# Kernel optimization log

Measured on AMD Instinct MI355X. Metric: run time of the kernel, lower is better.

## Reference

```python
import jax, jax.numpy as jnp
import numpy as np

N = 21  # nodes per graph (20 laser sectors + 1 robot node)
MAX_RANGE = 10.0
_bound = np.linspace(-np.pi / 2 - 0.03, np.pi / 2, 21, dtype=np.float32)[:-1]
_angles = _bound + np.float32(np.pi / 20)
ANGLE_FEAT = jnp.asarray(np.stack([np.sin(_angles), np.cos(_angles)], 1), dtype=jnp.float32)  # [20,2]


def _build_nodes(state24):
    # state24: [B,24] -> node features [B,21,7]
    B = state24.shape[0]
    laser = state24[:, :20, None] / MAX_RANGE                       # [B,20,1]
    angle = jnp.broadcast_to(ANGLE_FEAT[None], (B, 20, 2))          # [B,20,2]
    sector = jnp.concatenate([laser, angle, jnp.zeros((B, 20, 4), state24.dtype)], -1)  # [B,20,7]
    robot = jnp.concatenate([jnp.zeros((B, 1, 3), state24.dtype), state24[:, None, 20:]], -1)  # [B,1,7]
    return jnp.concatenate([sector, robot], axis=1)                 # [B,21,7]


def _gatv2(x, Wl, Wr, att, bias, heads, dim):
    # GATv2 over a fully-connected graph with self-loops (dense all-pairs).
    # e_ij = att . leaky_relu(Wl x_j + Wr x_i); alpha = softmax_j; out_i = sum_j alpha_ij (Wl x_j)
    B = x.shape[0]
    gl = (x @ Wl).reshape(B, N, heads, dim)  # source transform [B,j,H,D]
    gr = (x @ Wr).reshape(B, N, heads, dim)  # target transform [B,i,H,D]
    s = jax.nn.leaky_relu(gl[:, None] + gr[:, :, None], negative_slope=0.2)  # [B,i,j,H,D]
    e = jnp.einsum('bijhd,hd->bijh', s, att)                                  # [B,i,j,H]
    alpha = jax.nn.softmax(e, axis=2)                                          # softmax over sources j
    out = jnp.einsum('bijh,bjhd->bihd', alpha, gl).reshape(B, N, heads * dim)
    return out + bias


def setup_inputs() -> dict:
    key = jax.random.key(0)
    ks = jax.random.split(key, 16)
    r = lambda k, shape, s: (jax.random.normal(k, shape, dtype=jnp.float32) * s)
    B = 1024
    return {
        'state24': jax.random.normal(ks[0], (B, 24), dtype=jnp.float32),
        'Wl1': r(ks[1], (7, 256), 0.3), 'Wr1': r(ks[2], (7, 256), 0.3),
        'att1': r(ks[3], (4, 64), 0.1), 'b1': r(ks[4], (256,), 0.02),
        'Wl2': r(ks[5], (256, 64), 0.06), 'Wr2': r(ks[6], (256, 64), 0.06),
        'att2': r(ks[7], (1, 64), 0.1), 'b2': r(ks[8], (64,), 0.02),
        'fc1_w': r(ks[9], (64, 256), 0.12), 'fc1_b': r(ks[10], (256,), 0.02),
        'fc2_w': r(ks[11], (256, 256), 0.06), 'fc2_b': r(ks[12], (256,), 0.02),
        'fc3_w': r(ks[13], (256, 2), 0.06), 'fc3_b': r(ks[14], (2,), 0.02),
    }


def reference(state24, Wl1, Wr1, att1, b1, Wl2, Wr2, att2, b2,
              fc1_w, fc1_b, fc2_w, fc2_b, fc3_w, fc3_b):
    x = _build_nodes(state24)                               # [B,21,7]
    h = jax.nn.elu(_gatv2(x, Wl1, Wr1, att1, b1, 4, 64))    # [B,21,256]
    h = _gatv2(h, Wl2, Wr2, att2, b2, 1, 64)                # [B,21,64]
    nfv = jnp.mean(h, axis=1)                               # global_mean_pool -> [B,64]
    h = jax.nn.relu(nfv @ fc1_w + fc1_b)
    h = jax.nn.relu(h @ fc2_w + fc2_b)
    return jnp.tanh(h @ fc3_w + fc3_b)                      # [B,2]
```

## Files before the change

### kernel.cpp

```cpp
#include <hip/hip_runtime.h>
#include <hip/hip_fp16.h>
#include <math.h>

#define PI_D 3.141592653589793

typedef _Float16 h2 __attribute__((ext_vector_type(2)));
typedef _Float16 h4 __attribute__((ext_vector_type(4)));
typedef _Float16 h8 __attribute__((ext_vector_type(8)));
typedef unsigned short us8 __attribute__((ext_vector_type(8)));
typedef __fp16 f16v2 __attribute__((ext_vector_type(2)));
typedef __fp16 f16v8 __attribute__((ext_vector_type(8)));
typedef float f32x4 __attribute__((ext_vector_type(4)));

#define STR1 264
#define STR2H 72

#define SV(v, a, b) __builtin_shufflevector(v, v, a, b)

static __device__ __forceinline__ h2 pack_h2(float a, float b) {
    return __builtin_bit_cast(h2, __builtin_amdgcn_cvt_pkrtz(a, b));
}

static __device__ __forceinline__ float fdot2(h2 a, h2 b, float c) {
    return __builtin_amdgcn_fdot2(__builtin_bit_cast(f16v2, a),
                                  __builtin_bit_cast(f16v2, b), c, false);
}

static __device__ __forceinline__ h8 habs8(h8 x) {
    us8 u = __builtin_bit_cast(us8, x);
    us8 m = {0x7fff, 0x7fff, 0x7fff, 0x7fff, 0x7fff, 0x7fff, 0x7fff, 0x7fff};
    return __builtin_bit_cast(h8, (us8)(u & m));
}

static __device__ __forceinline__ f32x4 mfma16(h8 a, h8 b, f32x4 c) {
    return __builtin_amdgcn_mfma_f32_16x16x32_f16(
        __builtin_bit_cast(f16v8, a), __builtin_bit_cast(f16v8, b), c, 0, 0, 0);
}

static __device__ __forceinline__ void wave_fence() {
    asm volatile("" ::: "memory");
#if __has_builtin(__builtin_amdgcn_wave_barrier)
    __builtin_amdgcn_wave_barrier();
#endif
    asm volatile("" ::: "memory");
}

__global__ __launch_bounds__(256) void pack_weights_kernel(
    const float* __restrict__ Wl2, const float* __restrict__ Wr2,
    const float* __restrict__ fc1_w, const float* __restrict__ fc2_w,
    h8* __restrict__ ws)
{
    int idx = blockIdx.x * 256 + threadIdx.x;
    if (idx < 4096) {
        const float* W = idx < 2048 ? Wl2 : Wr2;
        int t = idx & 2047;
        int ntile = t >> 9, rem = t & 511;
        int kchunk = rem >> 6, lane = rem & 63;
        int n = ntile * 16 + (lane & 15);
        int k0 = kchunk * 32 + (lane >> 4) * 8;
        h8 o;
        #pragma unroll
        for (int j = 0; j < 8; ++j) o[j] = (_Float16)W[(k0 + j) * 64 + n];
        ws[idx] = o;
    } else if (idx < 6144) {
        int t = idx - 4096;
        int k2 = t >> 6, c = t & 63;
        h8 o;
        #pragma unroll
        for (int q = 0; q < 4; ++q) {
            o[2 * q]     = (_Float16)fc1_w[(2 * k2) * 256 + 4 * c + q];
            o[2 * q + 1] = (_Float16)fc1_w[(2 * k2 + 1) * 256 + 4 * c + q];
        }
        ws[idx] = o;
    } else {
        int t = idx - 6144;
        int k2 = t >> 6, c = t & 63;
        h8 o;
        #pragma unroll
        for (int q = 0; q < 4; ++q) {
            o[2 * q]     = (_Float16)fc2_w[(2 * k2) * 256 + 4 * c + q];
            o[2 * q + 1] = (_Float16)fc2_w[(2 * k2 + 1) * 256 + 4 * c + q];
        }
        ws[idx] = o;
    }
}

__global__ __launch_bounds__(256, 4) void actor_fused_kernel(
    const float* __restrict__ state24,
    const float* __restrict__ Wl1, const float* __restrict__ Wr1,
    const float* __restrict__ att1, const float* __restrict__ b1,
    const float* __restrict__ att2, const float* __restrict__ b2,
    const float* __restrict__ fc1_b, const float* __restrict__ fc2_b,
    const float* __restrict__ fc3_w, const float* __restrict__ fc3_b,
    const h8* __restrict__ wsL, const h8* __restrict__ wsR,
    const h8* __restrict__ wsF1, const h8* __restrict__ wsF2,
    float* __restrict__ out, int B)
{
    const int bix = blockIdx.x;
    if (bix >= B) return;
    const int tid = threadIdx.x;

    __shared__ float sinL[20], cosL[20], laserL[20], robotL[4];
    __shared__ __align__(16) h2 attLh[128];
    __shared__ __align__(16) h2 att2Lh[32];
    __shared__ __align__(16) _Float16 gr1h[22 * STR1];
    __shared__ __align__(16) union {
        struct { _Float16 gl1h[22 * STR1];
                 float ePf[128 * 24];
                 float uv[168]; } p1;
        struct { _Float16 gl2h[21 * STR2H];
                 _Float16 gr2h[21 * STR2H];
                 _Float16 gl2hT[64 * 32];
                 float e2[32 * 24];
                 float u2v2[42];
                 float red[4][256];
                 _Float16 nfvh[64]; _Float16 hah[256]; _Float16 hbh[256]; } p2;
    } U;

    if (tid < 20) {
        double step = (PI_D + 0.03) / 20.0;
        float bound = (float)(-PI_D / 2.0 - 0.03 + (double)tid * step);
        float ang = bound + (float)(PI_D / 20.0);
        sinL[tid] = sinf(ang);
        cosL[tid] = cosf(ang);
        laserL[tid] = state24[bix * 24 + tid] * 0.1f;
    }
    if (tid >= 32 && tid < 36) robotL[tid - 32] = state24[bix * 24 + 20 + (tid - 32)];
    if (tid < 128) {
        float2 ap = ((const float2*)att1)[tid];
        attLh[tid] = pack_h2(0.4f * ap.x, 0.4f * ap.y);
    }
    if (tid >= 128 && tid < 160) {
        float2 ap = ((const float2*)att2)[tid - 128];
        att2Lh[tid - 128] = pack_h2(0.4f * ap.x, 0.4f * ap.y);
    }
    __syncthreads();

    {
        const int h = tid >> 6;
        const int lane = tid & 63;

        {
            const int cp = lane & 31;
            const int half = lane >> 5;
            const int d2 = h * 32 + cp;
            float2 wl[7], wr[7];
            #pragma unroll
            for (int k = 0; k < 7; k++) {
                wl[k] = ((const float2*)Wl1)[k * 128 + d2];
                wr[k] = ((const float2*)Wr1)[k * 128 + d2];
            }
            if (half == 0) {
                h2 zz2 = {};
                ((h2*)(U.p1.gl1h + 21 * STR1))[d2] = zz2;
                ((h2*)(gr1h + 21 * STR1))[d2] = zz2;
            }
            const int base = half * 11;
            #pragma unroll
            for (int nn = 0; nn < 11; ++nn) {
                int node = base + nn;
                if (node < 21) {
                    float a0, a1, b0, b1v;
                    if (node < 20) {
                        float l = laserL[node], s = sinL[node], c = cosL[node];
                        a0 = l * wl[0].x + s * wl[1].x + c * wl[2].x;
                        a1 = l * wl[0].y + s * wl[1].y + c * wl[2].y;
                        b0 = l * wr[0].x + s * wr[1].x + c * wr[2].x;
                        b1v = l * wr[0].y + s * wr[1].y + c * wr[2].y;
                    } else {
                        float r0 = robotL[0], r1 = robotL[1], r2 = robotL[2], r3 = robotL[3];
                        a0 = r0 * wl[3].x + r1 * wl[4].x + r2 * wl[5].x + r3 * wl[6].x;
                        a1 = r0 * wl[3].y + r1 * wl[4].y + r2 * wl[5].y + r3 * wl[6].y;
                        b0 = r0 * wr[3].x + r1 * wr[4].x + r2 * wr[5].x + r3 * wr[6].x;
                        b1v = r0 * wr[3].y + r1 * wr[4].y + r2 * wr[5].y + r3 * wr[6].y;
                    }
                    ((h2*)(U.p1.gl1h + node * STR1))[d2] = pack_h2(a0, a1);
                    ((h2*)(gr1h + node * STR1))[d2] = pack_h2(b0, b1v);
                }
            }
        }
        wave_fence();

        {
            h2 ar[32];
            #pragma unroll
            for (int q = 0; q < 32; ++q) ar[q] = attLh[h * 32 + q];

            for (int it = 0; it < 7; ++it) {
                int q = it * 64 + lane;
                if (q < 441) {
                    int i = q / 21;
                    int j = q - i * 21;
                    const h8* gA8 = (const h8*)(U.p1.gl1h + j * STR1 + h * 64);
                    const h8* gB8 = (const h8*)(gr1h + i * STR1 + h * 64);
                    float m0 = 0.f, m1 = 0.f;
                    #pragma unroll
                    for (int ch = 0; ch < 8; ++ch) {
                        h8 x = gA8[ch] + gB8[ch];
                        h8 ax = habs8(x);
                        m0 = fdot2(SV(ax, 0, 1), ar[ch * 4 + 0], m0);
                        m1 = fdot2(SV(ax, 2, 3), ar[ch * 4 + 1], m1);
                        m0 = fdot2(SV(ax, 4, 5), ar[ch * 4 + 2], m0);
                        m1 = fdot2(SV(ax, 6, 7), ar[ch * 4 + 3], m1);
                    }
                    U.p1.ePf[(h * 32 + i) * 24 + j] = m0 + m1;
                }
            }
            if (lane < 42) {
                int isV = lane >= 21;
                int idx = isV ? lane - 21 : lane;
                const _Float16* rowp = (isV ? (const _Float16*)gr1h
                                            : (const _Float16*)U.p1.gl1h) + idx * STR1 + h * 64;
                const h8* row8 = (const h8*)rowp;
                float l0 = 0.f, l1 = 0.f;
                #pragma unroll
                for (int ch = 0; ch < 8; ++ch) {
                    h8 g = row8[ch];
                    l0 = fdot2(SV(g, 0, 1), ar[ch * 4 + 0], l0);
                    l1 = fdot2(SV(g, 2, 3), ar[ch * 4 + 1], l1);
                    l0 = fdot2(SV(g, 4, 5), ar[ch * 4 + 2], l0);
                    l1 = fdot2(SV(g, 6, 7), ar[ch * 4 + 3], l1);
                }
                U.p1.uv[(isV ? 84 : 0) + h * 21 + idx] = l0 + l1;
            }
        }
        wave_fence();

        if (lane < 21) {
            int r = h * 32 + lane;
            float* row = U.p1.ePf + r * 24;
            const float* uu = U.p1.uv + h * 21;
            float vi = 1.5f * U.p1.uv[84 + h * 21 + lane];
            float ebuf[21];
            float m = -1e30f;
            #pragma unroll
            for (int j = 0; j < 21; j++) {
                float e = row[j] + 1.5f * uu[j] + vi;
                ebuf[j] = e;
                m = fmaxf(m, e);
            }
            float s = 0.f;
            #pragma unroll
            for (int j = 0; j < 21; j++) { float v = __expf(ebuf[j] - m); ebuf[j] = v; s += v; }
            float rinv = 1.f / s;
            h8* hp8 = (h8*)(U.p1.ePf) + r * 6;
            h8 o0, o1, o2;
            #pragma unroll
            for (int q = 0; q < 8; ++q) o0[q] = (_Float16)(ebuf[q] * rinv);
            #pragma unroll
            for (int q = 0; q < 8; ++q) o1[q] = (_Float16)(ebuf[8 + q] * rinv);
            #pragma unroll
            for (int q = 0; q < 5; ++q) o2[q] = (_Float16)(ebuf[16 + q] * rinv);
            o2[5] = (_Float16)0.f; o2[6] = (_Float16)0.f; o2[7] = (_Float16)0.f;
            h8 zz = {};
            hp8[0] = o0; hp8[1] = o1; hp8[2] = o2;
            hp8[3] = zz; hp8[4] = zz; hp8[5] = zz;
        }
        {
            h8 zz = {};
            for (int z = lane; z < 66; z += 64) {
                int rr = z / 6, slot = z - rr * 6;
                ((h8*)U.p1.ePf)[(h * 32 + 21 + rr) * 6 + slot] = zz;
            }
        }
        wave_fence();

        {
            const int mcol = lane & 15;
            const int quad = lane >> 4;
            const h8* Af = (const h8*)U.p1.ePf;
            h8 A0 = Af[(h * 32 + mcol) * 6 + quad];
            h8 A1 = Af[(h * 32 + 16 + mcol) * 6 + quad];
            int rowoff[8];
            #pragma unroll
            for (int jj = 0; jj < 8; ++jj) {
                int rr = quad * 8 + jj;
                rowoff[jj] = (rr > 21 ? 21 : rr) * STR1;
            }
            const int colbase = h * 64 + mcol;
            f32x4 z4 = {0.f, 0.f, 0.f, 0.f};
            #pragma unroll
            for (int t = 0; t < 4; ++t) {
                int col = colbase + t * 16;
                h8 bv;
                #pragma unroll
                for (int jj = 0; jj < 8; ++jj) bv[jj] = U.p1.gl1h[rowoff[jj] + col];
                f32x4 d0 = mfma16(A0, bv, z4);
                f32x4 d1 = mfma16(A1, bv, z4);
                float bb = b1[col];
                #pragma unroll
                for (int r = 0; r < 4; ++r) {
                    int n0 = quad * 4 + r;
                    float v = d0[r] + bb;
                    v = v > 0.f ? v : __expf(v) - 1.f;
                    gr1h[n0 * STR1 + col] = (_Float16)v;
                    int n1 = 16 + quad * 4 + r;
                    if (n1 < 21) {
                        float w2 = d1[r] + bb;
                        w2 = w2 > 0.f ? w2 : __expf(w2) - 1.f;
                        gr1h[n1 * STR1 + col] = (_Float16)w2;
                    }
                }
            }
        }
    }
    __syncthreads();

    {
        const int lane = tid & 63;
        const int w = tid >> 6;
        const int mrow = lane & 15;
        const int quad = lane >> 4;
        int rowA1 = 16 + mrow; if (rowA1 > 21) rowA1 = 21;
        const h8* hA0 = (const h8*)(gr1h + mrow * STR1 + quad * 8);
        const h8* hA1 = (const h8*)(gr1h + rowA1 * STR1 + quad * 8);
        const h8* bL = wsL + w * 512 + lane;
        const h8* bR = wsR + w * 512 + lane;
        f32x4 aL0 = {0.f, 0.f, 0.f, 0.f}, aL1 = {0.f, 0.f, 0.f, 0.f};
        f32x4 aR0 = {0.f, 0.f, 0.f, 0.f}, aR1 = {0.f, 0.f, 0.f, 0.f};
        #pragma unroll
        for (int kc = 0; kc < 8; ++kc) {
            h8 A0 = hA0[kc * 4];
            h8 A1 = hA1[kc * 4];
            h8 BL = bL[kc * 64];
            h8 BR = bR[kc * 64];
            aL0 = mfma16(A0, BL, aL0);
            aL1 = mfma16(A1, BL, aL1);
            aR0 = mfma16(A0, BR, aR0);
            aR1 = mfma16(A1, BR, aR1);
        }
        const int col = w * 16 + mrow;
        #pragma unroll
        for (int r = 0; r < 4; ++r) {
            int row0 = quad * 4 + r;
            U.p2.gl2h[row0 * STR2H + col] = (_Float16)aL0[r];
            U.p2.gr2h[row0 * STR2H + col] = (_Float16)aR0[r];
            int row1 = 16 + row0;
            if (row1 < 21) {
                U.p2.gl2h[row1 * STR2H + col] = (_Float16)aL1[r];
                U.p2.gr2h[row1 * STR2H + col] = (_Float16)aR1[r];
            }
        }
        {
            h2 lo0 = pack_h2(aL0[0], aL0[1]);
            h2 hi0 = pack_h2(aL0[2], aL0[3]);
            h4 p0 = __builtin_shufflevector(lo0, hi0, 0, 1, 2, 3);
            *(h4*)(U.p2.gl2hT + col * 32 + quad * 4) = p0;
            h2 lo1 = pack_h2(aL1[0], aL1[1]);
            h2 hi1 = pack_h2(aL1[2], aL1[3]);
            h4 p1 = __builtin_shufflevector(lo1, hi1, 0, 1, 2, 3);
            *(h4*)(U.p2.gl2hT + col * 32 + 16 + quad * 4) = p1;
        }
    }
    __syncthreads();

    {
        h2 ar2[32];
        #pragma unroll
        for (int q = 0; q < 32; ++q) ar2[q] = att2Lh[q];

        #pragma unroll
        for (int it = 0; it < 2; ++it) {
            int t = it * 256 + tid;
            if (t < 441) {
                int i = t / 21;
                int j = t - i * 21;
                const h8* gA8 = (const h8*)(U.p2.gl2h + j * STR2H);
                const h8* gB8 = (const h8*)(U.p2.gr2h + i * STR2H);
                float m0 = 0.f, m1 = 0.f;
                #pragma unroll
                for (int ch = 0; ch < 8; ++ch) {
                    h8 x = gA8[ch] + gB8[ch];
                    h8 ax = habs8(x);
                    m0 = fdot2(SV(ax, 0, 1), ar2[ch * 4 + 0], m0);
                    m1 = fdot2(SV(ax, 2, 3), ar2[ch * 4 + 1], m1);
                    m0 = fdot2(SV(ax, 4, 5), ar2[ch * 4 + 2], m0);
                    m1 = fdot2(SV(ax, 6, 7), ar2[ch * 4 + 3], m1);
                }
                U.p2.e2[i * 24 + j] = m0 + m1;
            } else if (t < 483) {
                int u = t - 441;
                int r = u < 21 ? u : u - 21;
                const _Float16* rowp = (u < 21 ? U.p2.gl2h : U.p2.gr2h) + r * STR2H;
                const h8* row8 = (const h8*)rowp;
                float l0 = 0.f, l1 = 0.f;
                #pragma unroll
                for (int ch = 0; ch < 8; ++ch) {
                    h8 g = row8[ch];
                    l0 = fdot2(SV(g, 0, 1), ar2[ch * 4 + 0], l0);
                    l1 = fdot2(SV(g, 2, 3), ar2[ch * 4 + 1], l1);
                    l0 = fdot2(SV(g, 4, 5), ar2[ch * 4 + 2], l0);
                    l1 = fdot2(SV(g, 6, 7), ar2[ch * 4 + 3], l1);
                }
                U.p2.u2v2[u] = l0 + l1;
            }
        }
    }
    __syncthreads();

    if (tid < 21) {
        float* row = U.p2.e2 + tid * 24;
        const float* uu = U.p2.u2v2;
        float vi = 1.5f * U.p2.u2v2[21 + tid];
        float ebuf[21];
        float m = -1e30f;
        #pragma unroll
        for (int j = 0; j < 21; j++) {
            float e = row[j] + 1.5f * uu[j] + vi;
            ebuf[j] = e;
            m = fmaxf(m, e);
        }
        float s = 0.f;
        #pragma unroll
        for (int j = 0; j < 21; j++) { float v = __expf(ebuf[j] - m); ebuf[j] = v; s += v; }
        float rinv = 1.f / s;
        h8* hp8 = (h8*)(U.p2.e2) + tid * 6;
        h8 o0, o1, o2;
        #pragma unroll
        for (int q = 0; q < 8; ++q) o0[q] = (_Float16)(ebuf[q] * rinv);
        #pragma unroll
        for (int q = 0; q < 8; ++q) o1[q] = (_Float16)(ebuf[8 + q] * rinv);
        #pragma unroll
        for (int q = 0; q < 5; ++q) o2[q] = (_Float16)(ebuf[16 + q] * rinv);
        o2[5] = (_Float16)0.f; o2[6] = (_Float16)0.f; o2[7] = (_Float16)0.f;
        h8 zz = {};
        hp8[0] = o0; hp8[1] = o1; hp8[2] = o2;
        hp8[3] = zz; hp8[4] = zz; hp8[5] = zz;
    } else if (tid < 87) {
        int z = tid - 21;
        int rr = z / 6, slot = z - rr * 6;
        h8 zz = {};
        ((h8*)U.p2.e2)[(21 + rr) * 6 + slot] = zz;
    }
    __syncthreads();

    {
        const int lane = tid & 63;
        const int w = tid >> 6;
        const int mcol = lane & 15;
        const int quad = lane >> 4;
        const h8* Af2 = (const h8*)U.p2.e2;
        h8 A0 = Af2[mcol * 6 + quad];
        h8 A1 = Af2[(16 + mcol) * 6 + quad];
        h8 bv = *(const h8*)(U.p2.gl2hT + (w * 16 + mcol) * 32 + quad * 8);
        f32x4 z4 = {0.f, 0.f, 0.f, 0.f};
        f32x4 d0 = mfma16(A0, bv, z4);
        f32x4 d1 = mfma16(A1, bv, z4);
        float s = (d0[0] + d0[1]) + (d0[2] + d0[3])
                + (d1[0] + d1[1]) + (d1[2] + d1[3]);
        s += __shfl_xor(s, 16, 64);
        s += __shfl_xor(s, 32, 64);
        if (quad == 0) {
            int col = w * 16 + mcol;
            U.p2.nfvh[col] = (_Float16)(s * (1.f / 21.f) + b2[col]);
        }
    }
    __syncthreads();

    {
        int c = tid & 63, g = tid >> 6;
        const h2* x2p = (const h2*)U.p2.nfvh;
        float4 acc = {0.f, 0.f, 0.f, 0.f};
        #pragma unroll
        for (int kk = 0; kk < 8; ++kk) {
            int k2 = g * 8 + kk;
            h8 w = wsF1[k2 * 64 + c];
            h2 x2 = x2p[k2];
            acc.x = fdot2(SV(w, 0, 1), x2, acc.x);
            acc.y = fdot2(SV(w, 2, 3), x2, acc.y);
            acc.z = fdot2(SV(w, 4, 5), x2, acc.z);
            acc.w = fdot2(SV(w, 6, 7), x2, acc.w);
        }
        ((float4*)U.p2.red[g])[c] = acc;
    }
    __syncthreads();
    {
        float v = U.p2.red[0][tid] + U.p2.red[1][tid] + U.p2.red[2][tid] + U.p2.red[3][tid]
                  + fc1_b[tid];
        U.p2.hah[tid] = (_Float16)fmaxf(v, 0.f);
    }
    __syncthreads();

    {
        int c = tid & 63, g = tid >> 6;
        const h8* haH = (const h8*)U.p2.hah;
        float4 acc = {0.f, 0.f, 0.f, 0.f};
#define FC2_STEP(q, p)                                                          \
        {                                                                       \
            int k2 = g * 32 + (q) * 4 + (p);                                    \
            h8 w = wsF2[k2 * 64 + c];                                           \
            h2 x2 = __builtin_shufflevector(xa, xa, 2 * (p), 2 * (p) + 1);      \
            acc.x = fdot2(SV(w, 0, 1), x2, acc.x);                              \
            acc.y = fdot2(SV(w, 2, 3), x2, acc.y);                              \
            acc.z = fdot2(SV(w, 4, 5), x2, acc.z);                              \
            acc.w = fdot2(SV(w, 6, 7), x2, acc.w);                              \
        }
        #pragma unroll
        for (int q = 0; q < 8; ++q) {
            h8 xa = haH[g * 8 + q];
            FC2_STEP(q, 0)
            FC2_STEP(q, 1)
            FC2_STEP(q, 2)
            FC2_STEP(q, 3)
        }
#undef FC2_STEP
        ((float4*)U.p2.red[g])[c] = acc;
    }
    __syncthreads();
    {
        float v = U.p2.red[0][tid] + U.p2.red[1][tid] + U.p2.red[2][tid] + U.p2.red[3][tid]
                  + fc2_b[tid];
        U.p2.hbh[tid] = (_Float16)fmaxf(v, 0.f);
    }
    __syncthreads();

    if (tid < 128) {
        int o = tid >> 6, l = tid & 63;
        float s = 0.f;
        #pragma unroll
        for (int m = 0; m < 4; m++) {
            int k = l + 64 * m;
            s = fmaf((float)U.p2.hbh[k], fc3_w[k * 2 + o], s);
        }
        #pragma unroll
        for (int off = 32; off >= 1; off >>= 1) s += __shfl_down(s, off, 64);
        if (l == 0) out[bix * 2 + o] = tanhf(s + fc3_b[o]);
    }
}

extern "C" void kernel_launch(void* const* d_in, const int* in_sizes, int n_in,
                              void* d_out, int out_size, void* d_ws, size_t ws_size,
                              hipStream_t stream) {
    const float* state24 = (const float*)d_in[0];
    const float* Wl1 = (const float*)d_in[1];
    const float* Wr1 = (const float*)d_in[2];
    const float* att1 = (const float*)d_in[3];
    const float* b1 = (const float*)d_in[4];
    const float* Wl2 = (const float*)d_in[5];
    const float* Wr2 = (const float*)d_in[6];
    const float* att2 = (const float*)d_in[7];
    const float* b2 = (const float*)d_in[8];
    const float* fc1_w = (const float*)d_in[9];
    const float* fc1_b = (const float*)d_in[10];
    const float* fc2_w = (const float*)d_in[11];
    const float* fc2_b = (const float*)d_in[12];
    const float* fc3_w = (const float*)d_in[13];
    const float* fc3_b = (const float*)d_in[14];
    float* out = (float*)d_out;

    h8* ws = (h8*)d_ws;
    const h8* wsL = ws;
    const h8* wsR = ws + 2048;
    const h8* wsF1 = ws + 4096;
    const h8* wsF2 = ws + 6144;

    pack_weights_kernel<<<56, 256, 0, stream>>>(Wl2, Wr2, fc1_w, fc2_w, ws);

    int B = in_sizes[0] / 24;
    actor_fused_kernel<<<B, 256, 0, stream>>>(
        state24, Wl1, Wr1, att1, b1, att2, b2,
        fc1_b, fc2_b, fc3_w, fc3_b,
        wsL, wsR, wsF1, wsF2, out, B);
}
```

Before: 113.6 us.

## Process two samples per block to reuse weight loads across samples

Each block now handles two batch samples instead of one, so the grid is halved. Weight fragments for the layer-2 transforms and the FC layers are loaded once and applied to both samples, and barrier and setup costs are shared across the pair. In exchange, shared memory and register use per block roughly double, and launch bounds drop to 2 blocks per SM. With only 512 blocks the per-CU parallelism and occupancy fall, which may hurt latency hiding.

```diff
diff --git a/kernel.cpp b/kernel.cpp
--- a/kernel.cpp
+++ b/kernel.cpp
@@ -85,7 +85,7 @@
     }
 }
 
-__global__ __launch_bounds__(256, 4) void actor_fused_kernel(
+__global__ __launch_bounds__(256, 2) void actor_fused_kernel(
     const float* __restrict__ state24,
     const float* __restrict__ Wl1, const float* __restrict__ Wr1,
     const float* __restrict__ att1, const float* __restrict__ b1,
@@ -97,24 +97,26 @@
     float* __restrict__ out, int B)
 {
     const int bix = blockIdx.x;
-    if (bix >= B) return;
     const int tid = threadIdx.x;
-
-    __shared__ float sinL[20], cosL[20], laserL[20], robotL[4];
+    const int smp0 = 2 * bix;
+    if (smp0 >= B) return;
+    const int smp1 = (smp0 + 1 < B) ? smp0 + 1 : smp0;
+
+    __shared__ float sinL[20], cosL[20], laserL[2][20], robotL[2][4];
     __shared__ __align__(16) h2 attLh[128];
     __shared__ __align__(16) h2 att2Lh[32];
-    __shared__ __align__(16) _Float16 gr1h[22 * STR1];
+    __shared__ __align__(16) _Float16 gr1h[2][22 * STR1];
     __shared__ __align__(16) union {
-        struct { _Float16 gl1h[22 * STR1];
-                 float ePf[128 * 24];
-                 float uv[168]; } p1;
-        struct { _Float16 gl2h[21 * STR2H];
-                 _Float16 gr2h[21 * STR2H];
-                 _Float16 gl2hT[64 * 32];
-                 float e2[32 * 24];
-                 float u2v2[42];
-                 float red[4][256];
-                 _Float16 nfvh[64]; _Float16 hah[256]; _Float16 hbh[256]; } p2;
+        struct { _Float16 gl1h[2][22 * STR1];
+                 float ePf[2][128 * 24];
+                 float uv[2][168]; } p1;
+        struct { _Float16 gl2h[2][21 * STR2H];
+                 _Float16 gr2h[2][21 * STR2H];
+                 _Float16 gl2hT[2][64 * 32];
+                 float e2[2][32 * 24];
+                 float u2v2[2][42];
+                 float red[2][4][256];
+                 _Float16 nfvh[2][64]; _Float16 hah[2][256]; _Float16 hbh[2][256]; } p2;
     } U;
 
     if (tid < 20) {
@@ -123,9 +125,13 @@
         float ang = bound + (float)(PI_D / 20.0);
         sinL[tid] = sinf(ang);
         cosL[tid] = cosf(ang);
-        laserL[tid] = state24[bix * 24 + tid] * 0.1f;
-    }
-    if (tid >= 32 && tid < 36) robotL[tid - 32] = state24[bix * 24 + 20 + (tid - 32)];
+        laserL[0][tid] = state24[smp0 * 24 + tid] * 0.1f;
+        laserL[1][tid] = state24[smp1 * 24 + tid] * 0.1f;
+    }
+    if (tid >= 32 && tid < 40) {
+        int s = (tid - 32) >> 2, q = (tid - 32) & 3;
+        robotL[s][q] = state24[(s ? smp1 : smp0) * 24 + 20 + q];
+    }
     if (tid < 128) {
         float2 ap = ((const float2*)att1)[tid];
         attLh[tid] = pack_h2(0.4f * ap.x, 0.4f * ap.y);
@@ -152,30 +158,36 @@
             }
             if (half == 0) {
                 h2 zz2 = {};
-                ((h2*)(U.p1.gl1h + 21 * STR1))[d2] = zz2;
-                ((h2*)(gr1h + 21 * STR1))[d2] = zz2;
+                #pragma unroll
+                for (int s = 0; s < 2; ++s) {
+                    ((h2*)(U.p1.gl1h[s] + 21 * STR1))[d2] = zz2;
+                    ((h2*)(gr1h[s] + 21 * STR1))[d2] = zz2;
+                }
             }
             const int base = half * 11;
             #pragma unroll
             for (int nn = 0; nn < 11; ++nn) {
                 int node = base + nn;
                 if (node < 21) {
-                    float a0, a1, b0, b1v;
-                    if (node < 20) {
-                        float l = laserL[node], s = sinL[node], c = cosL[node];
-                        a0 = l * wl[0].x + s * wl[1].x + c * wl[2].x;
-                        a1 = l * wl[0].y + s * wl[1].y + c * wl[2].y;
-                        b0 = l * wr[0].x + s * wr[1].x + c * wr[2].x;
-                        b1v = l * wr[0].y + s * wr[1].y + c * wr[2].y;
-                    } else {
-                        float r0 = robotL[0], r1 = robotL[1], r2 = robotL[2], r3 = robotL[3];
-                        a0 = r0 * wl[3].x + r1 * wl[4].x + r2 * wl[5].x + r3 * wl[6].x;
-                        a1 = r0 * wl[3].y + r1 * wl[4].y + r2 * wl[5].y + r3 * wl[6].y;
-                        b0 = r0 * wr[3].x + r1 * wr[4].x + r2 * wr[5].x + r3 * wr[6].x;
-                        b1v = r0 * wr[3].y + r1 * wr[4].y + r2 * wr[5].y + r3 * wr[6].y;
+                    #pragma unroll
+                    for (int s = 0; s < 2; ++s) {
+                        float a0, a1, b0, b1v;
+                        if (node < 20) {
+                            float l = laserL[s][node], sv = sinL[node], c = cosL[node];
+                            a0 = l * wl[0].x + sv * wl[1].x + c * wl[2].x;
+                            a1 = l * wl[0].y + sv * wl[1].y + c * wl[2].y;
+                            b0 = l * wr[0].x + sv * wr[1].x + c * wr[2].x;
+                            b1v = l * wr[0].y + sv * wr[1].y + c * wr[2].y;
+                        } else {
+                            float r0 = robotL[s][0], r1 = robotL[s][1], r2 = robotL[s][2], r3 = robotL[s][3];
+                            a0 = r0 * wl[3].x + r1 * wl[4].x + r2 * wl[5].x + r3 * wl[6].x;
+                            a1 = r0 * wl[3].y + r1 * wl[4].y + r2 * wl[5].y + r3 * wl[6].y;
+                            b0 = r0 * wr[3].x + r1 * wr[4].x + r2 * wr[5].x + r3 * wr[6].x;
+                            b1v = r0 * wr[3].y + r1 * wr[4].y + r2 * wr[5].y + r3 * wr[6].y;
+                        }
+                        ((h2*)(U.p1.gl1h[s] + node * STR1))[d2] = pack_h2(a0, a1);
+                        ((h2*)(gr1h[s] + node * STR1))[d2] = pack_h2(b0, b1v);
                     }
-                    ((h2*)(U.p1.gl1h + node * STR1))[d2] = pack_h2(a0, a1);
-                    ((h2*)(gr1h + node * STR1))[d2] = pack_h2(b0, b1v);
                 }
             }
         }
@@ -186,51 +198,59 @@
             #pragma unroll
             for (int q = 0; q < 32; ++q) ar[q] = attLh[h * 32 + q];
 
-            for (int it = 0; it < 7; ++it) {
-                int q = it * 64 + lane;
-                if (q < 441) {
-                    int i = q / 21;
-                    int j = q - i * 21;
-                    const h8* gA8 = (const h8*)(U.p1.gl1h + j * STR1 + h * 64);
-                    const h8* gB8 = (const h8*)(gr1h + i * STR1 + h * 64);
-                    float m0 = 0.f, m1 = 0.f;
-                    #pragma unroll
-                    for (int ch = 0; ch < 8; ++ch) {
-                        h8 x = gA8[ch] + gB8[ch];
-                        h8 ax = habs8(x);
-                        m0 = fdot2(SV(ax, 0, 1), ar[ch * 4 + 0], m0);
-                        m1 = fdot2(SV(ax, 2, 3), ar[ch * 4 + 1], m1);
-                        m0 = fdot2(SV(ax, 4, 5), ar[ch * 4 + 2], m0);
-                        m1 = fdot2(SV(ax, 6, 7), ar[ch * 4 + 3], m1);
+            #pragma unroll
+            for (int s = 0; s < 2; ++s) {
+                for (int it = 0; it < 7; ++it) {
+                    int q = it * 64 + lane;
+                    if (q < 441) {
+                        int i = q / 21;
+                        int j = q - i * 21;
+                        const h8* gA8 = (const h8*)(U.p1.gl1h[s] + j * STR1 + h * 64);
+                        const h8* gB8 = (const h8*)(gr1h[s] + i * STR1 + h * 64);
+                        float m0 = 0.f, m1 = 0.f;
+                        #pragma unroll
+                        for (int ch = 0; ch < 8; ++ch) {
+                            h8 x = gA8[ch] + gB8[ch];
+                            h8 ax = habs8(x);
+                            m0 = fdot2(SV(ax, 0, 1), ar[ch * 4 + 0], m0);
+                            m1 = fdot2(SV(ax, 2, 3), ar[ch * 4 + 1], m1);
+                            m0 = fdot2(SV(ax, 4, 5), ar[ch * 4 + 2], m0);
+                            m1 = fdot2(SV(ax, 6, 7), ar[ch * 4 + 3], m1);
+                        }
+                        U.p1.ePf[s][(h * 32 + i) * 24 + j] = m0 + m1;
                     }
-                    U.p1.ePf[(h * 32 + i) * 24 + j] = m0 + m1;
                 }
             }
             if (lane < 42) {
                 int isV = lane >= 21;
                 int idx = isV ? lane - 21 : lane;
-                const _Float16* rowp = (isV ? (const _Float16*)gr1h
-                                            : (const _Float16*)U.p1.gl1h) + idx * STR1 + h * 64;
-                const h8* row8 = (const h8*)rowp;
-                float l0 = 0.f, l1 = 0.f;
                 #pragma unroll
-                for (int ch = 0; ch < 8; ++ch) {
-                    h8 g = row8[ch];
-                    l0 = fdot2(SV(g, 0, 1), ar[ch * 4 + 0], l0);
-                    l1 = fdot2(SV(g, 2, 3), ar[ch * 4 + 1], l1);
-                    l0 = fdot2(SV(g, 4, 5), ar[ch * 4 + 2], l0);
-                    l1 = fdot2(SV(g, 6, 7), ar[ch * 4 + 3], l1);
-                }
-                U.p1.uv[(isV ? 84 : 0) + h * 21 + idx] = l0 + l1;
+                for (int s = 0; s < 2; ++s) {
+                    const _Float16* rowp = (isV ? (const _Float16*)gr1h[s]
+                                                : (const _Float16*)U.p1.gl1h[s]) + idx * STR1 + h * 64;
+                    const h8* row8 = (const h8*)rowp;
+                    float l0 = 0.f, l1 = 0.f;
+                    #pragma unroll
+                    for (int ch = 0; ch < 8; ++ch) {
+                        h8 g = row8[ch];
+                        l0 = fdot2(SV(g, 0, 1), ar[ch * 4 + 0], l0);
+                        l1 = fdot2(SV(g, 2, 3), ar[ch * 4 + 1], l1);
+                        l0 = fdot2(SV(g, 4, 5), ar[ch * 4 + 2], l0);
+                        l1 = fdot2(SV(g, 6, 7), ar[ch * 4 + 3], l1);
+                    }
+                    U.p1.uv[s][(isV ? 84 : 0) + h * 21 + idx] = l0 + l1;
+                }
             }
         }
         wave_fence();
 
-        if (lane < 21) {
-            int r = h * 32 + lane;
-            float* row = U.p1.ePf + r * 24;
-            const float* uu = U.p1.uv + h * 21;
-            float vi = 1.5f * U.p1.uv[84 + h * 21 + lane];
+        if (lane < 42) {
+            int s = lane >= 21;
+            int i = lane - s * 21;
+            int r = h * 32 + i;
+            float* row = U.p1.ePf[s] + r * 24;
+            const float* uu = U.p1.uv[s] + h * 21;
+            float vi = 1.5f * U.p1.uv[s][84 + h * 21 + i];
             float ebuf[21];
             float m = -1e30f;
             #pragma unroll
@@ -239,11 +259,11 @@
                 ebuf[j] = e;
                 m = fmaxf(m, e);
             }
-            float s = 0.f;
-            #pragma unroll
-            for (int j = 0; j < 21; j++) { float v = __expf(ebuf[j] - m); ebuf[j] = v; s += v; }
-            float rinv = 1.f / s;
-            h8* hp8 = (h8*)(U.p1.ePf) + r * 6;
+            float sum = 0.f;
+            #pragma unroll
+            for (int j = 0; j < 21; j++) { float v = __expf(ebuf[j] - m); ebuf[j] = v; sum += v; }
+            float rinv = 1.f / sum;
+            h8* hp8 = (h8*)(U.p1.ePf[s]) + r * 6;
             h8 o0, o1, o2;
             #pragma unroll
             for (int q = 0; q < 8; ++q) o0[q] = (_Float16)(ebuf[q] * rinv);
@@ -258,9 +278,11 @@
         }
         {
             h8 zz = {};
-            for (int z = lane; z < 66; z += 64) {
-                int rr = z / 6, slot = z - rr * 6;
-                ((h8*)U.p1.ePf)[(h * 32 + 21 + rr) * 6 + slot] = zz;
+            for (int z = lane; z < 132; z += 64) {
+                int s = z >= 66;
+                int zz2 = z - s * 66;
+                int rr = zz2 / 6, slot = zz2 - rr * 6;
+                ((h8*)U.p1.ePf[s])[(h * 32 + 21 + rr) * 6 + slot] = zz;
             }
         }
         wave_fence();
@@ -268,9 +290,13 @@
         {
             const int mcol = lane & 15;
             const int quad = lane >> 4;
-            const h8* Af = (const h8*)U.p1.ePf;
-            h8 A0 = Af[(h * 32 + mcol) * 6 + quad];
-            h8 A1 = Af[(h * 32 + 16 + mcol) * 6 + quad];
+            h8 A0s[2], A1s[2];
+            #pragma unroll
+            for (int s = 0; s < 2; ++s) {
+                const h8* Af = (const h8*)U.p1.ePf[s];
+                A0s[s] = Af[(h * 32 + mcol) * 6 + quad];
+                A1s[s] = Af[(h * 32 + 16 + mcol) * 6 + quad];
+            }
             int rowoff[8];
             #pragma unroll
             for (int jj = 0; jj < 8; ++jj) {
@@ -282,23 +308,26 @@
             #pragma unroll
             for (int t = 0; t < 4; ++t) {
                 int col = colbase + t * 16;
-                h8 bv;
-                #pragma unroll
-                for (int jj = 0; jj < 8; ++jj) bv[jj] = U.p1.gl1h[rowoff[jj] + col];
-                f32x4 d0 = mfma16(A0, bv, z4);
-                f32x4 d1 = mfma16(A1, bv, z4);
                 float bb = b1[col];
                 #pragma unroll
-                for (int r = 0; r < 4; ++r) {
-                    int n0 = quad * 4 + r;
-                    float v = d0[r] + bb;
-                    v = v > 0.f ? v : __expf(v) - 1.f;
-                    gr1h[n0 * STR1 + col] = (_Float16)v;
-                    int n1 = 16 + quad * 4 + r;
-                    if (n1 < 21) {
-                        float w2 = d1[r] + bb;
-                        w2 = w2 > 0.f ? w2 : __expf(w2) - 1.f;
-                        gr1h[n1 * STR1 + col] = (_Float16)w2;
+                for (int s = 0; s < 2; ++s) {
+                    h8 bv;
+                    #pragma unroll
+                    for (int jj = 0; jj < 8; ++jj) bv[jj] = U.p1.gl1h[s][rowoff[jj] + col];
+                    f32x4 d0 = mfma16(A0s[s], bv, z4);
+                    f32x4 d1 = mfma16(A1s[s], bv, z4);
+                    #pragma unroll
+                    for (int r = 0; r < 4; ++r) {
+                        int n0 = quad * 4 + r;
+                        float v = d0[r] + bb;
+                        v = v > 0.f ? v : __expf(v) - 1.f;
+                        gr1h[s][n0 * STR1 + col] = (_Float16)v;
+                        int n1 = 16 + quad * 4 + r;
+                        if (n1 < 21) {
+                            float w2 = d1[r] + bb;
+                            w2 = w2 > 0.f ? w2 : __expf(w2) - 1.f;
+                            gr1h[s][n1 * STR1 + col] = (_Float16)w2;
+                        }
                     }
                 }
             }
@@ -312,44 +341,50 @@
         const int mrow = lane & 15;
         const int quad = lane >> 4;
         int rowA1 = 16 + mrow; if (rowA1 > 21) rowA1 = 21;
-        const h8* hA0 = (const h8*)(gr1h + mrow * STR1 + quad * 8);
-        const h8* hA1 = (const h8*)(gr1h + rowA1 * STR1 + quad * 8);
         const h8* bL = wsL + w * 512 + lane;
         const h8* bR = wsR + w * 512 + lane;
-        f32x4 aL0 = {0.f, 0.f, 0.f, 0.f}, aL1 = {0.f, 0.f, 0.f, 0.f};
-        f32x4 aR0 = {0.f, 0.f, 0.f, 0.f}, aR1 = {0.f, 0.f, 0.f, 0.f};
+        f32x4 aL0[2], aL1[2], aR0[2], aR1[2];
+        #pragma unroll
+        for (int s = 0; s < 2; ++s) {
+            aL0[s] = (f32x4){0.f, 0.f, 0.f, 0.f}; aL1[s] = (f32x4){0.f, 0.f, 0.f, 0.f};
+            aR0[s] = (f32x4){0.f, 0.f, 0.f, 0.f}; aR1[s] = (f32x4){0.f, 0.f, 0.f, 0.f};
+        }
         #pragma unroll
         for (int kc = 0; kc < 8; ++kc) {
-            h8 A0 = hA0[kc * 4];
-            h8 A1 = hA1[kc * 4];
             h8 BL = bL[kc * 64];
             h8 BR = bR[kc * 64];
-            aL0 = mfma16(A0, BL, aL0);
-            aL1 = mfma16(A1, BL, aL1);
-            aR0 = mfma16(A0, BR, aR0);
-            aR1 = mfma16(A1, BR, aR1);
+            #pragma unroll
+            for (int s = 0; s < 2; ++s) {
+                h8 A0 = *(const h8*)(gr1h[s] + mrow * STR1 + quad * 8 + kc * 32);
+                h8 A1 = *(const h8*)(gr1h[s] + rowA1 * STR1 + quad * 8 + kc * 32);
+                aL0[s] = mfma16(A0, BL, aL0[s]);
+                aL1[s] = mfma16(A1, BL, aL1[s]);
+                aR0[s] = mfma16(A0, BR, aR0[s]);
+                aR1[s] = mfma16(A1, BR, aR1[s]);
+            }
         }
         const int col = w * 16 + mrow;
         #pragma unroll
-        for (int r = 0; r < 4; ++r) {
-            int row0 = quad * 4 + r;
-            U.p2.gl2h[row0 * STR2H + col] = (_Float16)aL0[r];
-            U.p2.gr2h[row0 * STR2H + col] = (_Float16)aR0[r];
-            int row1 = 16 + row0;
-            if (row1 < 21) {
-                U.p2.gl2h[row1 * STR2H + col] = (_Float16)aL1[r];
-                U.p2.gr2h[row1 * STR2H + col] = (_Float16)aR1[r];
-            }
-        }
-        {
-            h2 lo0 = pack_h2(aL0[0], aL0[1]);
-            h2 hi0 = pack_h2(aL0[2], aL0[3]);
+        for (int s = 0; s < 2; ++s) {
+            #pragma unroll
+            for (int r = 0; r < 4; ++r) {
+                int row0 = quad * 4 + r;
+                U.p2.gl2h[s][row0 * STR2H + col] = (_Float16)aL0[s][r];
+                U.p2.gr2h[s][row0 * STR2H + col] = (_Float16)aR0[s][r];
+                int row1 = 16 + row0;
+                if (row1 < 21) {
+                    U.p2.gl2h[s][row1 * STR2H + col] = (_Float16)aL1[s][r];
+                    U.p2.gr2h[s][row1 * STR2H + col] = (_Float16)aR1[s][r];
+                }
+            }
+            h2 lo0 = pack_h2(aL0[s][0], aL0[s][1]);
+            h2 hi0 = pack_h2(aL0[s][2], aL0[s][3]);
             h4 p0 = __builtin_shufflevector(lo0, hi0, 0, 1, 2, 3);
-            *(h4*)(U.p2.gl2hT + col * 32 + quad * 4) = p0;
-            h2 lo1 = pack_h2(aL1[0], aL1[1]);
-            h2 hi1 = pack_h2(aL1[2], aL1[3]);
+            *(h4*)(U.p2.gl2hT[s] + col * 32 + quad * 4) = p0;
+            h2 lo1 = pack_h2(aL1[s][0], aL1[s][1]);
+            h2 hi1 = pack_h2(aL1[s][2], aL1[s][3]);
             h4 p1 = __builtin_shufflevector(lo1, hi1, 0, 1, 2, 3);
-            *(h4*)(U.p2.gl2hT + col * 32 + 16 + quad * 4) = p1;
+            *(h4*)(U.p2.gl2hT[s] + col * 32 + 16 + quad * 4) = p1;
         }
     }
     __syncthreads();
@@ -360,13 +395,15 @@
         for (int q = 0; q < 32; ++q) ar2[q] = att2Lh[q];
 
         #pragma unroll
-        for (int it = 0; it < 2; ++it) {
+        for (int it = 0; it < 4; ++it) {
             int t = it * 256 + tid;
-            if (t < 441) {
-                int i = t / 21;
-                int j = t - i * 21;
-                const h8* gA8 = (const h8*)(U.p2.gl2h + j * STR2H);
-                const h8* gB8 = (const h8*)(U.p2.gr2h + i * STR2H);
+            if (t < 882) {
+                int s = t >= 441;
+                int p = t - s * 441;
+                int i = p / 21;
+                int j = p - i * 21;
+                const h8* gA8 = (const h8*)(U.p2.gl2h[s] + j * STR2H);
+                const h8* gB8 = (const h8*)(U.p2.gr2h[s] + i * STR2H);
                 float m0 = 0.f, m1 = 0.f;
                 #pragma unroll
                 for (int ch = 0; ch < 8; ++ch) {
@@ -377,11 +414,14 @@
                     m0 = fdot2(SV(ax, 4, 5), ar2[ch * 4 + 2], m0);
                     m1 = fdot2(SV(ax, 6, 7), ar2[ch * 4 + 3], m1);
                 }
-                U.p2.e2[i * 24 + j] = m0 + m1;
-            } else if (t < 483) {
-                int u = t - 441;
-                int r = u < 21 ? u : u - 21;
-                const _Float16* rowp = (u < 21 ? U.p2.gl2h : U.p2.gr2h) + r * STR2H;
+                U.p2.e2[s][i * 24 + j] = m0 + m1;
+            } else if (t < 966) {
+                int u = t - 882;
+                int s = u >= 42;
+                int r = u - s * 42;
+                int isV = r >= 21;
+                int idx = r - isV * 21;
+                const _Float16* rowp = (isV ? U.p2.gr2h[s] : U.p2.gl2h[s]) + idx * STR2H;
                 const h8* row8 = (const h8*)rowp;
                 float l0 = 0.f, l1 = 0.f;
                 #pragma unroll
@@ -392,16 +432,18 @@
                     l0 = fdot2(SV(g, 4, 5), ar2[ch * 4 + 2], l0);
                     l1 = fdot2(SV(g, 6, 7), ar2[ch * 4 + 3], l1);
                 }
-                U.p2.u2v2[u] = l0 + l1;
-            }
-        }
-    }
-    __syncthreads();
-
-    if (tid < 21) {
-        float* row = U.p2.e2 + tid * 24;
-        const float* uu = U.p2.u2v2;
-        float vi = 1.5f * U.p2.u2v2[21 + tid];
+                U.p2.u2v2[s][isV * 21 + idx] = l0 + l1;
+            }
+        }
+    }
+    __syncthreads();
+
+    if (tid < 42) {
+        int s = tid >= 21;
+        int i = tid - s * 21;
+        float* row = U.p2.e2[s] + i * 24;
+        const float* uu = U.p2.u2v2[s];
+        float vi = 1.5f * U.p2.u2v2[s][21 + i];
         float ebuf[21];
         float m = -1e30f;
         #pragma unroll
@@ -410,11 +452,11 @@
             ebuf[j] = e;
             m = fmaxf(m, e);
         }
-        float s = 0.f;
-        #pragma unroll
-        for (int j = 0; j < 21; j++) { float v = __expf(ebuf[j] - m); ebuf[j] = v; s += v; }
-        float rinv = 1.f / s;
-        h8* hp8 = (h8*)(U.p2.e2) + tid * 6;
+        float sum = 0.f;
+        #pragma unroll
+        for (int j = 0; j < 21; j++) { float v = __expf(ebuf[j] - m); ebuf[j] = v; sum += v; }
+        float rinv = 1.f / sum;
+        h8* hp8 = (h8*)(U.p2.e2[s]) + i * 6;
         h8 o0, o1, o2;
         #pragma unroll
         for (int q = 0; q < 8; ++q) o0[q] = (_Float16)(ebuf[q] * rinv);
@@ -426,11 +468,13 @@
         h8 zz = {};
         hp8[0] = o0; hp8[1] = o1; hp8[2] = o2;
         hp8[3] = zz; hp8[4] = zz; hp8[5] = zz;
-    } else if (tid < 87) {
-        int z = tid - 21;
-        int rr = z / 6, slot = z - rr * 6;
+    } else if (tid < 174) {
+        int z = tid - 42;
+        int s = z >= 66;
+        int zz2 = z - s * 66;
+        int rr = zz2 / 6, slot = zz2 - rr * 6;
         h8 zz = {};
-        ((h8*)U.p2.e2)[(21 + rr) * 6 + slot] = zz;
+        ((h8*)U.p2.e2[s])[(21 + rr) * 6 + slot] = zz;
     }
     __syncthreads();
 
@@ -439,92 +483,117 @@
         const int w = tid >> 6;
         const int mcol = lane & 15;
         const int quad = lane >> 4;
-        const h8* Af2 = (const h8*)U.p2.e2;
-        h8 A0 = Af2[mcol * 6 + quad];
-        h8 A1 = Af2[(16 + mcol) * 6 + quad];
-        h8 bv = *(const h8*)(U.p2.gl2hT + (w * 16 + mcol) * 32 + quad * 8);
+        const int col = w * 16 + mcol;
+        float bb = b2[col];
         f32x4 z4 = {0.f, 0.f, 0.f, 0.f};
-        f32x4 d0 = mfma16(A0, bv, z4);
-        f32x4 d1 = mfma16(A1, bv, z4);
-        float s = (d0[0] + d0[1]) + (d0[2] + d0[3])
-                + (d1[0] + d1[1]) + (d1[2] + d1[3]);
-        s += __shfl_xor(s, 16, 64);
-        s += __shfl_xor(s, 32, 64);
-        if (quad == 0) {
-            int col = w * 16 + mcol;
-            U.p2.nfvh[col] = (_Float16)(s * (1.f / 21.f) + b2[col]);
+        #pragma unroll
+        for (int s = 0; s < 2; ++s) {
+            const h8* Af2 = (const h8*)U.p2.e2[s];
+            h8 A0 = Af2[mcol * 6 + quad];
+            h8 A1 = Af2[(16 + mcol) * 6 + quad];
+            h8 bv = *(const h8*)(U.p2.gl2hT[s] + col * 32 + quad * 8);
+            f32x4 d0 = mfma16(A0, bv, z4);
+            f32x4 d1 = mfma16(A1, bv, z4);
+            float sum = (d0[0] + d0[1]) + (d0[2] + d0[3])
+                      + (d1[0] + d1[1]) + (d1[2] + d1[3]);
+            sum += __shfl_xor(sum, 16, 64);
+            sum += __shfl_xor(sum, 32, 64);
+            if (quad == 0) U.p2.nfvh[s][col] = (_Float16)(sum * (1.f / 21.f) + bb);
         }
     }
     __syncthreads();
 
     {
         int c = tid & 63, g = tid >> 6;
-        const h2* x2p = (const h2*)U.p2.nfvh;
-        float4 acc = {0.f, 0.f, 0.f, 0.f};
+        float4 acc0 = {0.f, 0.f, 0.f, 0.f}, acc1 = {0.f, 0.f, 0.f, 0.f};
         #pragma unroll
         for (int kk = 0; kk < 8; ++kk) {
             int k2 = g * 8 + kk;
             h8 w = wsF1[k2 * 64 + c];
-            h2 x2 = x2p[k2];
-            acc.x = fdot2(SV(w, 0, 1), x2, acc.x);
-            acc.y = fdot2(SV(w, 2, 3), x2, acc.y);
-            acc.z = fdot2(SV(w, 4, 5), x2, acc.z);
-            acc.w = fdot2(SV(w, 6, 7), x2, acc.w);
-        }
-        ((float4*)U.p2.red[g])[c] = acc;
-    }
-    __syncthreads();
-    {
-        float v = U.p2.red[0][tid] + U.p2.red[1][tid] + U.p2.red[2][tid] + U.p2.red[3][tid]
-                  + fc1_b[tid];
-        U.p2.hah[tid] = (_Float16)fmaxf(v, 0.f);
+            h2 x0 = ((const h2*)U.p2.nfvh[0])[k2];
+            h2 x1 = ((const h2*)U.p2.nfvh[1])[k2];
+            acc0.x = fdot2(SV(w, 0, 1), x0, acc0.x);
+            acc0.y = fdot2(SV(w, 2, 3), x0, acc0.y);
+            acc0.z = fdot2(SV(w, 4, 5), x0, acc0.z);
+            acc0.w = fdot2(SV(w, 6, 7), x0, acc0.w);
+            acc1.x = fdot2(SV(w, 0, 1), x1, acc1.x);
+            acc1.y = fdot2(SV(w, 2, 3), x1, acc1.y);
+            acc1.z = fdot2(SV(w, 4, 5), x1, acc1.z);
+            acc1.w = fdot2(SV(w, 6, 7), x1, acc1.w);
+        }
+        ((float4*)U.p2.red[0][g])[c] = acc0;
+        ((float4*)U.p2.red[1][g])[c] = acc1;
+    }
+    __syncthreads();
+    {
+        float bb = fc1_b[tid];
+        #pragma unroll
+        for (int s = 0; s < 2; ++s) {
+            float v = U.p2.red[s][0][tid] + U.p2.red[s][1][tid]
+                    + U.p2.red[s][2][tid] + U.p2.red[s][3][tid] + bb;
+            U.p2.hah[s][tid] = (_Float16)fmaxf(v, 0.f);
+        }
     }
     __syncthreads();
 
     {
         int c = tid & 63, g = tid >> 6;
-        const h8* haH = (const h8*)U.p2.hah;
-        float4 acc = {0.f, 0.f, 0.f, 0.f};
+        const h8* ha0 = (const h8*)U.p2.hah[0];
+        const h8* ha1 = (const h8*)U.p2.hah[1];
+        float4 acc0 = {0.f, 0.f, 0.f, 0.f}, acc1 = {0.f, 0.f, 0.f, 0.f};
 #define FC2_STEP(q, p)                                                          \
         {                                                                       \
             int k2 = g * 32 + (q) * 4 + (p);                                    \
             h8 w = wsF2[k2 * 64 + c];                                           \
-            h2 x2 = __builtin_shufflevector(xa, xa, 2 * (p), 2 * (p) + 1);      \
-            acc.x = fdot2(SV(w, 0, 1), x2, acc.x);                              \
-            acc.y = fdot2(SV(w, 2, 3), x2, acc.y);                              \
-            acc.z = fdot2(SV(w, 4, 5), x2, acc.z);                              \
-            acc.w = fdot2(SV(w, 6, 7), x2, acc.w);                              \
+            h2 x0 = __builtin_shufflevector(xa0, xa0, 2 * (p), 2 * (p) + 1);    \
+            h2 x1 = __builtin_shufflevector(xa1, xa1, 2 * (p), 2 * (p) + 1);    \
+            acc0.x = fdot2(SV(w, 0, 1), x0, acc0.x);                            \
+            acc0.y = fdot2(SV(w, 2, 3), x0, acc0.y);                            \
+            acc0.z = fdot2(SV(w, 4, 5), x0, acc0.z);                            \
+            acc0.w = fdot2(SV(w, 6, 7), x0, acc0.w);                            \
+            acc1.x = fdot2(SV(w, 0, 1), x1, acc1.x);                            \
+            acc1.y = fdot2(SV(w, 2, 3), x1, acc1.y);                            \
+            acc1.z = fdot2(SV(w, 4, 5), x1, acc1.z);                            \
+            acc1.w = fdot2(SV(w, 6, 7), x1, acc1.w);                            \
         }
         #pragma unroll
         for (int q = 0; q < 8; ++q) {
-            h8 xa = haH[g * 8 + q];
+            h8 xa0 = ha0[g * 8 + q];
+            h8 xa1 = ha1[g * 8 + q];
             FC2_STEP(q, 0)
             FC2_STEP(q, 1)
             FC2_STEP(q, 2)
             FC2_STEP(q, 3)
         }
 #undef FC2_STEP
-        ((float4*)U.p2.red[g])[c] = acc;
-    }
-    __syncthreads();
-    {
-        float v = U.p2.red[0][tid] + U.p2.red[1][tid] + U.p2.red[2][tid] + U.p2.red[3][tid]
-                  + fc2_b[tid];
-        U.p2.hbh[tid] = (_Float16)fmaxf(v, 0.f);
-    }
-    __syncthreads();
-
-    if (tid < 128) {
-        int o = tid >> 6, l = tid & 63;
-        float s = 0.f;
+        ((float4*)U.p2.red[0][g])[c] = acc0;
+        ((float4*)U.p2.red[1][g])[c] = acc1;
+    }
+    __syncthreads();
+    {
+        float bb = fc2_b[tid];
+        #pragma unroll
+        for (int s = 0; s < 2; ++s) {
+            float v = U.p2.red[s][0][tid] + U.p2.red[s][1][tid]
+                    + U.p2.red[s][2][tid] + U.p2.red[s][3][tid] + bb;
+            U.p2.hbh[s][tid] = (_Float16)fmaxf(v, 0.f);
+        }
+    }
+    __syncthreads();
+
+    {
+        int g = tid >> 6;
+        int o = g & 1, s = g >> 1;
+        int l = tid & 63;
+        float sum = 0.f;
         #pragma unroll
         for (int m = 0; m < 4; m++) {
             int k = l + 64 * m;
-            s = fmaf((float)U.p2.hbh[k], fc3_w[k * 2 + o], s);
-        }
-        #pragma unroll
-        for (int off = 32; off >= 1; off >>= 1) s += __shfl_down(s, off, 64);
-        if (l == 0) out[bix * 2 + o] = tanhf(s + fc3_b[o]);
+            sum = fmaf((float)U.p2.hbh[s][k], fc3_w[k * 2 + o], sum);
+        }
+        #pragma unroll
+        for (int off = 32; off >= 1; off >>= 1) sum += __shfl_down(sum, off, 64);
+        if (l == 0 && smp0 + s < B) out[(smp0 + s) * 2 + o] = tanhf(sum + fc3_b[o]);
     }
 }
 
@@ -557,7 +626,8 @@
     pack_weights_kernel<<<56, 256, 0, stream>>>(Wl2, Wr2, fc1_w, fc2_w, ws);
 
     int B = in_sizes[0] / 24;
-    actor_fused_kernel<<<B, 256, 0, stream>>>(
+    int nb = (B + 1) / 2;
+    actor_fused_kernel<<<nb, 256, 0, stream>>>(
         state24, Wl1, Wr1, att1, b1, att2, b2,
         fc1_b, fc2_b, fc3_w, fc3_b,
         wsL, wsR, wsF1, wsF2, out, B);
```

New measurement: 111.7 us, median of 2. Within noise of the previous version (-1.7%).
